# Performance work log

Measured on AMD Instinct MI355X. Metric: run time of the kernel, lower is better.

## Reference

```python
import jax, jax.numpy as jnp
import numpy as np

P = 7            # pooling_size
SCALE = 1.0 / 16  # spatial_scale


def _roi_align(feat, tf):
    # feat: [B,C,T,H,W] (L2-normalized), tf: [N,7] = [b, x1, y1, t1, x2, y2, t2]
    # RoIAlignAvg with temporal pooled size == T (identity in time): bilinear
    # sample at each spatial bin center for every frame.
    H, W = feat.shape[-2], feat.shape[-1]
    b = tf[:, 0].astype(jnp.int32)
    x1, y1 = tf[:, 1] * SCALE, tf[:, 2] * SCALE
    x2, y2 = tf[:, 4] * SCALE, tf[:, 5] * SCALE
    bw = jnp.maximum(x2 - x1 + SCALE, 1e-3) / P
    bh = jnp.maximum(y2 - y1 + SCALE, 1e-3) / P
    ctr = jnp.arange(P, dtype=feat.dtype) + 0.5
    xs = jnp.clip(x1[:, None] + ctr * bw[:, None], 0.0, W - 1)  # [N,P]
    ys = jnp.clip(y1[:, None] + ctr * bh[:, None], 0.0, H - 1)  # [N,P]
    x0 = jnp.floor(xs); y0 = jnp.floor(ys)
    fx = xs - x0; fy = ys - y0
    x0i = x0.astype(jnp.int32); x1i = jnp.minimum(x0i + 1, W - 1)
    y0i = y0.astype(jnp.int32); y1i = jnp.minimum(y0i + 1, H - 1)

    def g(yi, xi):
        # advanced indices broadcast to [N,P,P]; result [N,P,P,C,T]
        return feat[b[:, None, None], :, :, yi[:, :, None], xi[:, None, :]]

    wy0 = (1 - fy)[:, :, None, None, None]; wy1 = fy[:, :, None, None, None]
    wx0 = (1 - fx)[:, None, :, None, None]; wx1 = fx[:, None, :, None, None]
    out = (wy0 * wx0 * g(y0i, x0i) + wy0 * wx1 * g(y0i, x1i)
           + wy1 * wx0 * g(y1i, x0i) + wy1 * wx1 * g(y1i, x1i))
    return jnp.transpose(out, (0, 3, 4, 1, 2))  # [N,C,T,P,P]


def _forward(base_feat, tubes, gt_rois, gt_tubes, conv_w, conv_b, w1, b1, w2, b2, wp, bp):
    B, C, T = base_feat.shape[:3]
    R = tubes.shape[1]
    # F.normalize(base_feat, p=2, dim=1)
    feat = base_feat / jnp.maximum(
        jnp.linalg.norm(base_feat, axis=1, keepdims=True), 1e-12)

    # --- ragged scatter: rois[b,i,t1:t2+1,1:] = tubes[b,i,[1,2,4,5]] ---
    f = jnp.arange(T)
    f_off = (f[None, :] + jnp.arange(B)[:, None] * T).astype(tubes.dtype)  # [B,T]
    t1 = tubes[..., 3].astype(jnp.int32)[..., None]
    t2 = tubes[..., 6].astype(jnp.int32)[..., None]
    mask = (f[None, None, :] >= t1) & (f[None, None, :] <= t2)  # [B,R,T]
    box = tubes[..., jnp.array([1, 2, 4, 5])]                   # [B,R,4]
    rois_box = jnp.where(mask[..., None], box[:, :, None, :],
                         jnp.zeros((), tubes.dtype))
    rois = jnp.concatenate(
        [jnp.broadcast_to(f_off[:, None, :, None], (B, R, T, 1)), rois_box], -1)

    # --- RoIAlign + AvgPool3d over T + head (eval mode: dropout = identity) ---
    pooled = _roi_align(feat, tubes.reshape(-1, 7))  # [N,C,T,P,P]
    pooled = pooled.mean(axis=2)                     # [N,C,P,P]
    x = jnp.einsum('nchw,oc->nohw', pooled, conv_w) + conv_b[None, :, None, None]
    x = x.reshape(x.shape[0], -1)                    # [N, C*P*P]
    x = jax.nn.relu(x @ w1 + b1)
    x = jax.nn.relu(x @ w2 + b2)
    bbox_pred = x @ wp + bp                          # [N, 4*T]
    return bbox_pred, pooled, rois


def setup_inputs() -> dict:
    B, R, T, C, HF, IMG = 4, 64, 16, 256, 14, 224
    ks = jax.random.split(jax.random.key(0), 16)
    base_feat = jax.random.normal(ks[0], (B, C, T, HF, HF), jnp.float32)
    x1 = jax.random.uniform(ks[1], (B, R), minval=0.0, maxval=IMG / 2)
    y1 = jax.random.uniform(ks[2], (B, R), minval=0.0, maxval=IMG / 2)
    x2 = jnp.minimum(x1 + jax.random.uniform(ks[3], (B, R), minval=16.0, maxval=IMG / 2), IMG - 1.0)
    y2 = jnp.minimum(y1 + jax.random.uniform(ks[4], (B, R), minval=16.0, maxval=IMG / 2), IMG - 1.0)
    tt = jax.random.randint(ks[5], (B, R, 2), 0, T)
    t1 = jnp.min(tt, -1).astype(jnp.float32)
    t2 = jnp.max(tt, -1).astype(jnp.float32)
    bidx = jnp.broadcast_to(jnp.arange(B)[:, None], (B, R)).astype(jnp.float32)
    tubes = jnp.stack([bidx, x1, y1, t1, x2, y2, t2], -1)
    s = 0.02
    return {
        'base_feat': base_feat,
        'tubes': tubes,
        'gt_rois': jax.random.normal(ks[6], (B, 10, T, 5), jnp.float32),
        'gt_tubes': jax.random.normal(ks[7], (B, 10, 7), jnp.float32),
        'conv_w': jax.random.normal(ks[8], (C, C), jnp.float32) * s,
        'conv_b': jnp.zeros((C,), jnp.float32),
        'w1': jax.random.normal(ks[9], (C * P * P, 2048), jnp.float32) * s,
        'b1': jnp.zeros((2048,), jnp.float32),
        'w2': jax.random.normal(ks[10], (2048, 512), jnp.float32) * s,
        'b2': jnp.zeros((512,), jnp.float32),
        'wp': jax.random.normal(ks[11], (512, 4 * T), jnp.float32) * s,
        'bp': jnp.zeros((4 * T,), jnp.float32),
    }


def reference(base_feat, tubes, gt_rois, gt_tubes, conv_w, conv_b, w1, b1, w2, b2, wp, bp):
    return _forward(base_feat, tubes, gt_rois, gt_tubes, conv_w, conv_b, w1, b1, w2, b2, wp, bp)
```

## Files before the change

kernel.cpp:

```cpp
#include <hip/hip_runtime.h>

#define HH 14
#define WW 14
#define HWSZ 196
#define TT 16
#define CC 256
#define BB 4
#define RR 64
#define NROI 256
#define PP 7
#define PP2 49

typedef short s4v __attribute__((ext_vector_type(4)));
typedef short s8v __attribute__((ext_vector_type(8)));
typedef float f4v __attribute__((ext_vector_type(4)));

__device__ inline ushort f2bf(float f) {
    union { float f; unsigned u; } v; v.f = f;
    unsigned r = v.u + 0x7fffu + ((v.u >> 16) & 1u);
    return (ushort)(r >> 16);
}

__global__ void k_sumsq(const float* __restrict__ base, float* __restrict__ partial) {
    int blk = blockIdx.x;
    int bt = blk >> 3, cg = blk & 7;
    int hw = threadIdx.x;
    if (hw >= HWSZ) return;
    int b = bt >> 4, t = bt & 15;
    const float* p = base + ((size_t)(b * CC + cg * 32) * TT + t) * HWSZ + hw;
    float s = 0.f;
    #pragma unroll 8
    for (int c = 0; c < 32; ++c) {
        float v = p[(size_t)c * TT * HWSZ];
        s += v * v;
    }
    partial[cg * 12544 + bt * HWSZ + hw] = s;
}

__global__ void k_finish_inv(const float* __restrict__ partial, float* __restrict__ inv) {
    int j = blockIdx.x * 256 + threadIdx.x;
    if (j >= 12544) return;
    float s = 0.f;
    #pragma unroll
    for (int cg = 0; cg < 8; ++cg) s += partial[cg * 12544 + j];
    inv[j] = 1.0f / fmaxf(sqrtf(s), 1e-12f);
}

__global__ void k_tsum(const float* __restrict__ base, const float* __restrict__ inv,
                       float* __restrict__ tsum) {
    int bc = blockIdx.x;
    int hw = threadIdx.x;
    if (hw >= HWSZ) return;
    int b = bc >> 8;
    const float* p = base + (size_t)bc * TT * HWSZ + hw;
    const float* iv = inv + b * TT * HWSZ + hw;
    float s = 0.f;
    #pragma unroll
    for (int t = 0; t < TT; ++t) s += p[t * HWSZ] * iv[t * HWSZ];
    tsum[(size_t)bc * HWSZ + hw] = s;
}

__global__ void k_rois(const float* __restrict__ tubes, float* __restrict__ rois) {
    int idx = blockIdx.x * 256 + threadIdx.x;
    if (idx >= BB * RR * TT) return;
    int t = idx & 15;
    int br = idx >> 4;
    int b = br >> 6;
    const float* tb = tubes + br * 7;
    int t1 = (int)tb[3], t2 = (int)tb[6];
    bool m = (t >= t1) && (t <= t2);
    float* o = rois + (size_t)idx * 5;
    o[0] = (float)(b * TT + t);
    o[1] = m ? tb[1] : 0.f;
    o[2] = m ? tb[2] : 0.f;
    o[3] = m ? tb[4] : 0.f;
    o[4] = m ? tb[5] : 0.f;
}

__global__ void k_roialign(const float* __restrict__ tubes, const float* __restrict__ tsum,
                           float* __restrict__ pooled, float* __restrict__ pooledT) {
    __shared__ int sx0[PP], sx1[PP], sy0[PP], sy1[PP];
    __shared__ float sfx[PP], sfy[PP];
    __shared__ int sb;
    int n = blockIdx.x;
    int tid = threadIdx.x;
    if (tid < PP) {
        const float* tb = tubes + n * 7;
        float x1 = tb[1] * 0.0625f, y1 = tb[2] * 0.0625f;
        float x2 = tb[4] * 0.0625f, y2 = tb[5] * 0.0625f;
        float bw = fmaxf(x2 - x1 + 0.0625f, 0.001f) * (1.0f / PP);
        float bh = fmaxf(y2 - y1 + 0.0625f, 0.001f) * (1.0f / PP);
        float ctr = tid + 0.5f;
        float xs = fminf(fmaxf(x1 + ctr * bw, 0.f), (float)(WW - 1));
        float ys = fminf(fmaxf(y1 + ctr * bh, 0.f), (float)(HH - 1));
        float x0f = floorf(xs), y0f = floorf(ys);
        int x0 = (int)x0f, y0 = (int)y0f;
        sx0[tid] = x0; sx1[tid] = min(x0 + 1, WW - 1);
        sy0[tid] = y0; sy1[tid] = min(y0 + 1, HH - 1);
        sfx[tid] = xs - x0f; sfy[tid] = ys - y0f;
        if (tid == 0) sb = (int)tb[0];
    }
    __syncthreads();
    const float* tbase = tsum + (size_t)sb * CC * HWSZ;
    for (int idx = tid; idx < CC * PP2; idx += 256) {
        int c = idx / PP2, bin = idx % PP2;
        int py = bin / PP, px = bin % PP;
        const float* tp = tbase + (size_t)c * HWSZ;
        float fx = sfx[px], fy = sfy[py];
        int y0 = sy0[py] * WW, y1 = sy1[py] * WW;
        float v00 = tp[y0 + sx0[px]];
        float v01 = tp[y0 + sx1[px]];
        float v10 = tp[y1 + sx0[px]];
        float v11 = tp[y1 + sx1[px]];
        float v = (1.f - fy) * ((1.f - fx) * v00 + fx * v01)
                + fy        * ((1.f - fx) * v10 + fx * v11);
        v *= (1.0f / TT);
        pooled[(size_t)n * CC * PP2 + idx] = v;
        pooledT[((size_t)n * PP2 + bin) * CC + c] = v;
    }
}

__global__ __launch_bounds__(256) void gemm64(const float* __restrict__ A,
                                              const float* __restrict__ B_,
                                              float* __restrict__ Cp,
                                              int M, int N, int K,
                                              int lda, int ldb, int kChunk) {
    __shared__ float As[16][64];
    __shared__ float Bs[16][68];
    int m0 = blockIdx.x * 64, n0 = blockIdx.y * 64;
    int s = blockIdx.z;
    int k0 = s * kChunk, kend = k0 + kChunk;
    int tid = threadIdx.x;
    int am = tid >> 2, ak = (tid & 3) << 2;
    int bk = tid >> 4, bn = (tid & 15) << 2;
    int tm = tid >> 4, tn = tid & 15;
    float acc[4][4] = {};
    const float* Aptr = A + (size_t)(m0 + am) * lda + ak;
    const float* Bptr = B_ + (size_t)bk * ldb + n0 + bn;

    for (int kk = k0; kk < kend; kk += 16) {
        float4 av = *(const float4*)(Aptr + kk);
        float4 bv = *(const float4*)(Bptr + (size_t)kk * ldb);
        __syncthreads();
        As[ak + 0][am] = av.x;
        As[ak + 1][am] = av.y;
        As[ak + 2][am] = av.z;
        As[ak + 3][am] = av.w;
        *(float4*)&Bs[bk][bn] = bv;
        __syncthreads();
        #pragma unroll
        for (int k = 0; k < 16; ++k) {
            float4 a = *(const float4*)&As[k][tm << 2];
            float4 b = *(const float4*)&Bs[k][tn << 2];
            float a4[4] = {a.x, a.y, a.z, a.w};
            float b4[4] = {b.x, b.y, b.z, b.w};
            #pragma unroll
            for (int i = 0; i < 4; ++i)
                #pragma unroll
                for (int j = 0; j < 4; ++j)
                    acc[i][j] += a4[i] * b4[j];
        }
    }
    float* Cs = Cp + (size_t)s * M * N;
    #pragma unroll
    for (int i = 0; i < 4; ++i) {
        float4 v = make_float4(acc[i][0], acc[i][1], acc[i][2], acc[i][3]);
        *(float4*)&Cs[(size_t)(m0 + (tm << 2) + i) * N + n0 + (tn << 2)] = v;
    }
}

__global__ void k_reduce(const float* __restrict__ part, const float* __restrict__ bias,
                         float* __restrict__ out, int MN, int N, int S, int relu) {
    int idx = blockIdx.x * 256 + threadIdx.x;
    if (idx >= MN) return;
    float s = bias[idx % N];
    for (int i = 0; i < S; ++i) s += part[(size_t)i * MN + idx];
    if (relu) s = fmaxf(s, 0.f);
    out[idx] = s;
}

__global__ __launch_bounds__(512) void conv_mfma(const float* __restrict__ pooledT,
                                                 const float* __restrict__ conv_w,
                                                 const float* __restrict__ conv_b,
                                                 float* __restrict__ x) {
    __shared__ __align__(16) ushort Ab[2][8192];
    __shared__ __align__(16) ushort Bres[8192];
    const int m0 = blockIdx.x * 256, o0 = blockIdx.y * 64;
    const int tid = threadIdx.x;
    const int lane = tid & 63, w = tid >> 6;
    const int wm = w & 3, wn = w >> 2;
    const int fr = lane & 15, fg = lane >> 4;

    for (int ii = tid; ii < 2048; ii += 512) {
        int o_l = ii >> 5, cq = ii & 31;
        const float* s = conv_w + (size_t)(o0 + o_l) * 256 + cq * 8;
        float4 v0 = *(const float4*)s;
        float4 v1 = *(const float4*)(s + 4);
        float vv[8] = {v0.x, v0.y, v0.z, v0.w, v1.x, v1.y, v1.z, v1.w};
        int dbase = (cq >> 2) * 2048 + (o_l >> 4) * 512 + (cq & 3) * 128 + (o_l & 15);
        #pragma unroll
        for (int jc = 0; jc < 8; ++jc) Bres[dbase + jc * 16] = f2bf(vv[jc]);
    }

    int ii0 = tid, ii1 = 512 + tid, ii2 = 1024 + tid, ii3 = 1536 + tid;
    const float* pA0 = pooledT + (size_t)(m0 + (ii0 >> 3)) * 256 + (ii0 & 7) * 4;
    const float* pA1 = pooledT + (size_t)(m0 + (ii1 >> 3)) * 256 + (ii1 & 7) * 4;
    const float* pA2 = pooledT + (size_t)(m0 + (ii2 >> 3)) * 256 + (ii2 & 7) * 4;
    const float* pA3 = pooledT + (size_t)(m0 + (ii3 >> 3)) * 256 + (ii3 & 7) * 4;
#define CDOFF(ii) (((ii >> 3) >> 4) * 512 + ((ii & 7) >> 1) * 128 + ((ii >> 3) & 15) * 8 + (ii & 1) * 4)
    const int do0 = CDOFF(ii0), do1 = CDOFF(ii1), do2 = CDOFF(ii2), do3 = CDOFF(ii3);
#undef CDOFF
    float4 a0_, a1_, a2_, a3_;
#define CONV_LOAD(t) do { a0_ = *(const float4*)(pA0 + (t) * 32); \
                          a1_ = *(const float4*)(pA1 + (t) * 32); \
                          a2_ = *(const float4*)(pA2 + (t) * 32); \
                          a3_ = *(const float4*)(pA3 + (t) * 32); } while (0)
#define W4(dst, v) do { s4v _u; _u[0]=(short)f2bf((v).x); _u[1]=(short)f2bf((v).y); \
                        _u[2]=(short)f2bf((v).z); _u[3]=(short)f2bf((v).w); \
                        *(s4v*)(dst) = _u; } while (0)
#define CONV_WRITE(buf) do { W4(Ab[buf] + do0, a0_); W4(Ab[buf] + do1, a1_); \
                             W4(Ab[buf] + do2, a2_); W4(Ab[buf] + do3, a3_); } while (0)

    CONV_LOAD(0);
    CONV_WRITE(0);
    __syncthreads();

    const int aoff = wm * 2048 + fg * 128 + fr * 8;
    f4v acc[4][2];
    #pragma unroll
    for (int i = 0; i < 4; ++i)
        #pragma unroll
        for (int j = 0; j < 2; ++j) acc[i][j] = (f4v){0.f, 0.f, 0.f, 0.f};

    for (int t = 0; t < 8; ++t) {
        if (t < 7) CONV_LOAD(t + 1);
        const ushort* A = Ab[t & 1];
        s8v a0 = *(const s8v*)(A + aoff);
        s8v a1 = *(const s8v*)(A + aoff + 512);
        s8v a2 = *(const s8v*)(A + aoff + 1024);
        s8v a3 = *(const s8v*)(A + aoff + 1536);
        unsigned bbase = (unsigned)(size_t)(&Bres[0]) + t * 4096 + wn * 2048 + fg * 256 + fr * 2;
        s4v bl0, bh0, bl1, bh1;
        asm volatile("ds_read_b64_tr_b16 %0, %2\n\t"
                     "ds_read_b64_tr_b16 %1, %2 offset:128"
                     : "=v"(bl0), "=v"(bh0) : "v"(bbase));
        asm volatile("ds_read_b64_tr_b16 %0, %2 offset:1024\n\t"
                     "ds_read_b64_tr_b16 %1, %2 offset:1152"
                     : "=v"(bl1), "=v"(bh1) : "v"(bbase));
        asm volatile("s_waitcnt lgkmcnt(0)" ::: "memory");
        __builtin_amdgcn_sched_barrier(0);
        s8v b0, b1;
        b0[0] = bl0[0]; b0[1] = bl0[1]; b0[2] = bl0[2]; b0[3] = bl0[3];
        b0[4] = bh0[0]; b0[5] = bh0[1]; b0[6] = bh0[2]; b0[7] = bh0[3];
        b1[0] = bl1[0]; b1[1] = bl1[1]; b1[2] = bl1[2]; b1[3] = bl1[3];
        b1[4] = bh1[0]; b1[5] = bh1[1]; b1[6] = bh1[2]; b1[7] = bh1[3];
        acc[0][0] = __builtin_amdgcn_mfma_f32_16x16x32_bf16(a0, b0, acc[0][0], 0, 0, 0);
        acc[0][1] = __builtin_amdgcn_mfma_f32_16x16x32_bf16(a0, b1, acc[0][1], 0, 0, 0);
        acc[1][0] = __builtin_amdgcn_mfma_f32_16x16x32_bf16(a1, b0, acc[1][0], 0, 0, 0);
        acc[1][1] = __builtin_amdgcn_mfma_f32_16x16x32_bf16(a1, b1, acc[1][1], 0, 0, 0);
        acc[2][0] = __builtin_amdgcn_mfma_f32_16x16x32_bf16(a2, b0, acc[2][0], 0, 0, 0);
        acc[2][1] = __builtin_amdgcn_mfma_f32_16x16x32_bf16(a2, b1, acc[2][1], 0, 0, 0);
        acc[3][0] = __builtin_amdgcn_mfma_f32_16x16x32_bf16(a3, b0, acc[3][0], 0, 0, 0);
        acc[3][1] = __builtin_amdgcn_mfma_f32_16x16x32_bf16(a3, b1, acc[3][1], 0, 0, 0);
        if (t < 7) CONV_WRITE((t + 1) & 1);
        __syncthreads();
    }
#undef CONV_LOAD
#undef CONV_WRITE
#undef W4

    #pragma unroll
    for (int ni = 0; ni < 2; ++ni) {
        int o = o0 + wn * 32 + ni * 16 + fr;
        float cb = conv_b[o];
        #pragma unroll
        for (int mi = 0; mi < 4; ++mi)
            #pragma unroll
            for (int i = 0; i < 4; ++i) {
                int gm = m0 + wm * 64 + mi * 16 + fg * 4 + i;
                int n = gm / 49;
                int hw = gm - n * 49;
                x[(size_t)n * 12544 + o * 49 + hw] = acc[mi][ni][i] + cb;
            }
    }
}

__global__ void k_cvt_x(const float* __restrict__ x, ushort* __restrict__ xb) {
    int idx = blockIdx.x * 256 + threadIdx.x;
    if (idx >= 256 * 1568) return;
    int kg = idx >> 10;
    int r = idx & 1023;
    int rblk = r >> 6, q = (r >> 4) & 3, fr = r & 15;
    int m = rblk * 16 + fr;
    const float* src = x + (size_t)m * 12544 + kg * 32 + q * 8;
    float4 v0 = *(const float4*)src;
    float4 v1 = *(const float4*)(src + 4);
    ushort o[8] = {f2bf(v0.x), f2bf(v0.y), f2bf(v0.z), f2bf(v0.w),
                   f2bf(v1.x), f2bf(v1.y), f2bf(v1.z), f2bf(v1.w)};
    *(s8v*)(xb + (size_t)idx * 8) = *(s8v*)o;
}

__global__ __launch_bounds__(512) void fc1_mfma(const ushort* __restrict__ xb,
                                                const float* __restrict__ w1,
                                                float* __restrict__ part) {
    __shared__ __align__(16) ushort Ab[4][8192];
    __shared__ __align__(16) ushort Bbf[2][2048];
    const int nblk = blockIdx.x, s = blockIdx.y;
    const int n0 = nblk * 64;
    const int k0 = s * 1568;
    const int tid = threadIdx.x;
    const int lane = tid & 63, w = tid >> 6;
    const int wm = w & 3, wn = w >> 2;
    const int fr = lane & 15, fg = lane >> 4;

    const ushort* gA = xb + (size_t)s * 49 * 8192;
    const int slot0 = tid, slot1 = 512 + tid;

    const int kr = (w >> 2) * 16 + (lane >> 2);
    const int bnb = w & 3, bnq = lane & 3;
    const float* gB = w1 + (size_t)(k0 + kr) * 2048 + n0 + bnb * 16 + bnq * 4;
    const int bw_u = bnb * 512 + kr * 16 + bnq * 4;

    const int aoff = wm * 2048 + fg * 128 + fr * 8;
    f4v acc[4][2];
    #pragma unroll
    for (int i = 0; i < 4; ++i)
        #pragma unroll
        for (int j = 0; j < 2; ++j) acc[i][j] = (f4v){0.f, 0.f, 0.f, 0.f};

#define STAGE_A(buf, kg) do {                                                                   \
    ushort* _d = Ab[buf];                                                                       \
    __builtin_amdgcn_global_load_lds(                                                           \
        (const __attribute__((address_space(1))) void*)(gA + (size_t)(kg) * 8192 + slot0 * 8),  \
        (__attribute__((address_space(3))) void*)(_d + slot0 * 8), 16, 0, 0);                   \
    __builtin_amdgcn_global_load_lds(                                                           \
        (const __attribute__((address_space(1))) void*)(gA + (size_t)(kg) * 8192 + slot1 * 8),  \
        (__attribute__((address_space(3))) void*)(_d + slot1 * 8), 16, 0, 0);                   \
} while (0)
#define GBP(t) (*(const float4*)(gB + (size_t)(t) * 65536))
#define BWRITE(buf, rb) do {                                                                    \
    s4v _u; _u[0] = (short)f2bf((rb).x); _u[1] = (short)f2bf((rb).y);                           \
    _u[2] = (short)f2bf((rb).z); _u[3] = (short)f2bf((rb).w);                                   \
    *(s4v*)&Bbf[buf][bw_u] = _u;                                                                \
} while (0)

    float4 rb0, rb1, rb2, rb3;
    STAGE_A(0, 0);
    STAGE_A(1, 1);
    rb0 = GBP(0); rb1 = GBP(1); rb2 = GBP(2); rb3 = GBP(3);
    BWRITE(0, rb0);
    __builtin_amdgcn_sched_barrier(0);
    asm volatile("s_waitcnt vmcnt(3) lgkmcnt(0)" ::: "memory");
    __builtin_amdgcn_s_barrier();
    __builtin_amdgcn_sched_barrier(0);

#define FC1_BODY(t, rbL, rbU) do {                                                              \
    int kg2 = (t) + 2 > 48 ? 48 : (t) + 2;                                                      \
    int kg4 = (t) + 4 > 48 ? 48 : (t) + 4;                                                      \
    STAGE_A(((t) + 2) & 3, kg2);                                                                \
    __builtin_amdgcn_sched_barrier(0);                                                          \
    rbL = GBP(kg4);                                                                             \
    __builtin_amdgcn_sched_barrier(0);                                                          \
    const ushort* _A = Ab[(t) & 3];                                                             \
    s8v _a0 = *(const s8v*)(_A + aoff);                                                         \
    s8v _a1 = *(const s8v*)(_A + aoff + 512);                                                   \
    s8v _a2 = *(const s8v*)(_A + aoff + 1024);                                                  \
    s8v _a3 = *(const s8v*)(_A + aoff + 1536);                                                  \
    unsigned _bb = (unsigned)(size_t)(&Bbf[(t) & 1][0]) + wn * 2048 + fg * 256 + fr * 2;        \
    s4v _bl0, _bh0, _bl1, _bh1;                                                                 \
    asm volatile("ds_read_b64_tr_b16 %0, %2\n\t"                                                \
                 "ds_read_b64_tr_b16 %1, %2 offset:128"                                         \
                 : "=v"(_bl0), "=v"(_bh0) : "v"(_bb));                                          \
    asm volatile("ds_read_b64_tr_b16 %0, %2 offset:1024\n\t"                                    \
                 "ds_read_b64_tr_b16 %1, %2 offset:1152"                                        \
                 : "=v"(_bl1), "=v"(_bh1) : "v"(_bb));                                          \
    asm volatile("s_waitcnt lgkmcnt(0)" ::: "memory");                                          \
    __builtin_amdgcn_sched_barrier(0);                                                          \
    s8v _b0, _b1;                                                                               \
    _b0[0]=_bl0[0]; _b0[1]=_bl0[1]; _b0[2]=_bl0[2]; _b0[3]=_bl0[3];                             \
    _b0[4]=_bh0[0]; _b0[5]=_bh0[1]; _b0[6]=_bh0[2]; _b0[7]=_bh0[3];                             \
    _b1[0]=_bl1[0]; _b1[1]=_bl1[1]; _b1[2]=_bl1[2]; _b1[3]=_bl1[3];                             \
    _b1[4]=_bh1[0]; _b1[5]=_bh1[1]; _b1[6]=_bh1[2]; _b1[7]=_bh1[3];                             \
    acc[0][0] = __builtin_amdgcn_mfma_f32_16x16x32_bf16(_a0, _b0, acc[0][0], 0, 0, 0);          \
    acc[0][1] = __builtin_amdgcn_mfma_f32_16x16x32_bf16(_a0, _b1, acc[0][1], 0, 0, 0);          \
    acc[1][0] = __builtin_amdgcn_mfma_f32_16x16x32_bf16(_a1, _b0, acc[1][0], 0, 0, 0);          \
    acc[1][1] = __builtin_amdgcn_mfma_f32_16x16x32_bf16(_a1, _b1, acc[1][1], 0, 0, 0);          \
    acc[2][0] = __builtin_amdgcn_mfma_f32_16x16x32_bf16(_a2, _b0, acc[2][0], 0, 0, 0);          \
    acc[2][1] = __builtin_amdgcn_mfma_f32_16x16x32_bf16(_a2, _b1, acc[2][1], 0, 0, 0);          \
    acc[3][0] = __builtin_amdgcn_mfma_f32_16x16x32_bf16(_a3, _b0, acc[3][0], 0, 0, 0);          \
    acc[3][1] = __builtin_amdgcn_mfma_f32_16x16x32_bf16(_a3, _b1, acc[3][1], 0, 0, 0);          \
    BWRITE(((t) + 1) & 1, rbU);                                                                 \
    __builtin_amdgcn_sched_barrier(0);                                                          \
    asm volatile("s_waitcnt vmcnt(4) lgkmcnt(0)" ::: "memory");                                 \
    __builtin_amdgcn_s_barrier();                                                               \
    __builtin_amdgcn_sched_barrier(0);                                                          \
} while (0)

    for (int tb = 0; tb < 44; tb += 4) {
        FC1_BODY(tb + 0, rb0, rb1);
        FC1_BODY(tb + 1, rb1, rb2);
        FC1_BODY(tb + 2, rb2, rb3);
        FC1_BODY(tb + 3, rb3, rb0);
    }
    FC1_BODY(44, rb0, rb1);
    FC1_BODY(45, rb1, rb2);
    FC1_BODY(46, rb2, rb3);
    FC1_BODY(47, rb3, rb0);

    {
        const ushort* _A = Ab[0];
        s8v _a0 = *(const s8v*)(_A + aoff);
        s8v _a1 = *(const s8v*)(_A + aoff + 512);
        s8v _a2 = *(const s8v*)(_A + aoff + 1024);
        s8v _a3 = *(const s8v*)(_A + aoff + 1536);
        unsigned _bb = (unsigned)(size_t)(&Bbf[0][0]) + wn * 2048 + fg * 256 + fr * 2;
        s4v _bl0, _bh0, _bl1, _bh1;
        asm volatile("ds_read_b64_tr_b16 %0, %2\n\t"
                     "ds_read_b64_tr_b16 %1, %2 offset:128"
                     : "=v"(_bl0), "=v"(_bh0) : "v"(_bb));
        asm volatile("ds_read_b64_tr_b16 %0, %2 offset:1024\n\t"
                     "ds_read_b64_tr_b16 %1, %2 offset:1152"
                     : "=v"(_bl1), "=v"(_bh1) : "v"(_bb));
        asm volatile("s_waitcnt lgkmcnt(0)" ::: "memory");
        __builtin_amdgcn_sched_barrier(0);
        s8v _b0, _b1;
        _b0[0]=_bl0[0]; _b0[1]=_bl0[1]; _b0[2]=_bl0[2]; _b0[3]=_bl0[3];
        _b0[4]=_bh0[0]; _b0[5]=_bh0[1]; _b0[6]=_bh0[2]; _b0[7]=_bh0[3];
        _b1[0]=_bl1[0]; _b1[1]=_bl1[1]; _b1[2]=_bl1[2]; _b1[3]=_bl1[3];
        _b1[4]=_bh1[0]; _b1[5]=_bh1[1]; _b1[6]=_bh1[2]; _b1[7]=_bh1[3];
        acc[0][0] = __builtin_amdgcn_mfma_f32_16x16x32_bf16(_a0, _b0, acc[0][0], 0, 0, 0);
        acc[0][1] = __builtin_amdgcn_mfma_f32_16x16x32_bf16(_a0, _b1, acc[0][1], 0, 0, 0);
        acc[1][0] = __builtin_amdgcn_mfma_f32_16x16x32_bf16(_a1, _b0, acc[1][0], 0, 0, 0);
        acc[1][1] = __builtin_amdgcn_mfma_f32_16x16x32_bf16(_a1, _b1, acc[1][1], 0, 0, 0);
        acc[2][0] = __builtin_amdgcn_mfma_f32_16x16x32_bf16(_a2, _b0, acc[2][0], 0, 0, 0);
        acc[2][1] = __builtin_amdgcn_mfma_f32_16x16x32_bf16(_a2, _b1, acc[2][1], 0, 0, 0);
        acc[3][0] = __builtin_amdgcn_mfma_f32_16x16x32_bf16(_a3, _b0, acc[3][0], 0, 0, 0);
        acc[3][1] = __builtin_amdgcn_mfma_f32_16x16x32_bf16(_a3, _b1, acc[3][1], 0, 0, 0);
    }
#undef FC1_BODY
#undef STAGE_A
#undef GBP
#undef BWRITE

    float* dst = part + (size_t)s * 256 * 2048 + n0 + wn * 32 + fr;
    #pragma unroll
    for (int mi = 0; mi < 4; ++mi)
        #pragma unroll
        for (int ni = 0; ni < 2; ++ni)
            #pragma unroll
            for (int i = 0; i < 4; ++i) {
                int row = wm * 64 + mi * 16 + fg * 4 + i;
                dst[(size_t)row * 2048 + ni * 16] = acc[mi][ni][i];
            }
}

extern "C" void kernel_launch(void* const* d_in, const int* in_sizes, int n_in,
                              void* d_out, int out_size, void* d_ws, size_t ws_size,
                              hipStream_t stream) {
    const float* base   = (const float*)d_in[0];
    const float* tubes  = (const float*)d_in[1];
    const float* conv_w = (const float*)d_in[4];
    const float* conv_b = (const float*)d_in[5];
    const float* w1     = (const float*)d_in[6];
    const float* b1     = (const float*)d_in[7];
    const float* w2     = (const float*)d_in[8];
    const float* b2     = (const float*)d_in[9];
    const float* wp     = (const float*)d_in[10];
    const float* bp     = (const float*)d_in[11];

    float* out    = (float*)d_out;
    float* bbox   = out;
    float* pooled = out + 16384;
    float* rois   = out + 16384 + 3211264;

    float* ws      = (float*)d_ws;
    float* inv     = ws;
    float* partial = ws + 12544;
    float* tsum    = ws + 112896;
    float* pooledT = ws + 313600;
    float* x       = ws + 3524864;
    float* h1      = ws + 6736128;
    float* h2      = ws + 7260416;
    float* part    = ws + 7391488;
    ushort* xb     = (ushort*)pooledT;

    k_sumsq<<<BB * TT * 8, 256, 0, stream>>>(base, partial);
    k_finish_inv<<<49, 256, 0, stream>>>(partial, inv);
    k_tsum<<<BB * CC, 256, 0, stream>>>(base, inv, tsum);
    k_rois<<<(BB * RR * TT + 255) / 256, 256, 0, stream>>>(tubes, rois);
    k_roialign<<<NROI, 256, 0, stream>>>(tubes, tsum, pooled, pooledT);

    conv_mfma<<<dim3(49, 4), 512, 0, stream>>>(pooledT, conv_w, conv_b, x);

    k_cvt_x<<<1568, 256, 0, stream>>>(x, xb);

    fc1_mfma<<<dim3(32, 8), 512, 0, stream>>>(xb, w1, part);
    k_reduce<<<(256 * 2048 + 255) / 256, 256, 0, stream>>>(part, b1, h1, 256 * 2048, 2048, 8, 1);

    gemm64<<<dim3(4, 8, 8), 256, 0, stream>>>(h1, w2, part,
                                              256, 512, 2048, 2048, 512, 256);
    k_reduce<<<(256 * 512 + 255) / 256, 256, 0, stream>>>(part, b2, h2, 256 * 512, 512, 8, 1);

    gemm64<<<dim3(4, 1, 8), 256, 0, stream>>>(h2, wp, part,
                                              256, 64, 512, 512, 64, 64);
    k_reduce<<<(256 * 64 + 255) / 256, 256, 0, stream>>>(part, bp, bbox, 256 * 64, 64, 8, 0);
}
```

Before: 133.3 us.

## Fuse rois into roialign, write bf16 fc1 operand from conv, drop k_cvt_x

The rois scatter moves into the RoIAlign kernel, and RoIAlign splits its work into two loops so that both the pooled and pooledT stores are coalesced. The conv epilogue writes bf16 directly in the fc1 operand layout, ordered hw-major. fc1 then gathers w1 rows with a matching permuted k index, which removes the separate conversion kernel and its fp32 intermediate round trip. fc1 grid axes are also swapped. The cost is a second bilinear pass in RoIAlign, scattered 2-byte stores in the conv epilogue, and noncontiguous w1 row reads in fc1.

```diff
diff --git a/kernel.cpp b/kernel.cpp
--- a/kernel.cpp
+++ b/kernel.cpp
@@ -60,25 +60,9 @@
     tsum[(size_t)bc * HWSZ + hw] = s;
 }
 
-__global__ void k_rois(const float* __restrict__ tubes, float* __restrict__ rois) {
-    int idx = blockIdx.x * 256 + threadIdx.x;
-    if (idx >= BB * RR * TT) return;
-    int t = idx & 15;
-    int br = idx >> 4;
-    int b = br >> 6;
-    const float* tb = tubes + br * 7;
-    int t1 = (int)tb[3], t2 = (int)tb[6];
-    bool m = (t >= t1) && (t <= t2);
-    float* o = rois + (size_t)idx * 5;
-    o[0] = (float)(b * TT + t);
-    o[1] = m ? tb[1] : 0.f;
-    o[2] = m ? tb[2] : 0.f;
-    o[3] = m ? tb[4] : 0.f;
-    o[4] = m ? tb[5] : 0.f;
-}
-
 __global__ void k_roialign(const float* __restrict__ tubes, const float* __restrict__ tsum,
-                           float* __restrict__ pooled, float* __restrict__ pooledT) {
+                           float* __restrict__ pooled, float* __restrict__ pooledT,
+                           float* __restrict__ rois) {
     __shared__ int sx0[PP], sx1[PP], sy0[PP], sy1[PP];
     __shared__ float sfx[PP], sfy[PP];
     __shared__ int sb;
@@ -100,11 +84,24 @@
         sfx[tid] = xs - x0f; sfy[tid] = ys - y0f;
         if (tid == 0) sb = (int)tb[0];
     }
+    if (tid < TT) {
+        const float* tb = tubes + n * 7;
+        int t1 = (int)tb[3], t2 = (int)tb[6];
+        bool m = (tid >= t1) && (tid <= t2);
+        int b = n >> 6;
+        float* o = rois + ((size_t)n * TT + tid) * 5;
+        o[0] = (float)(b * TT + tid);
+        o[1] = m ? tb[1] : 0.f;
+        o[2] = m ? tb[2] : 0.f;
+        o[3] = m ? tb[4] : 0.f;
+        o[4] = m ? tb[5] : 0.f;
+    }
     __syncthreads();
     const float* tbase = tsum + (size_t)sb * CC * HWSZ;
+
     for (int idx = tid; idx < CC * PP2; idx += 256) {
-        int c = idx / PP2, bin = idx % PP2;
-        int py = bin / PP, px = bin % PP;
+        int c = idx / PP2, bin = idx - (idx / PP2) * PP2;
+        int py = bin / PP, px = bin - (bin / PP) * PP;
         const float* tp = tbase + (size_t)c * HWSZ;
         float fx = sfx[px], fy = sfy[py];
         int y0 = sy0[py] * WW, y1 = sy1[py] * WW;
@@ -114,9 +111,21 @@
         float v11 = tp[y1 + sx1[px]];
         float v = (1.f - fy) * ((1.f - fx) * v00 + fx * v01)
                 + fy        * ((1.f - fx) * v10 + fx * v11);
-        v *= (1.0f / TT);
-        pooled[(size_t)n * CC * PP2 + idx] = v;
-        pooledT[((size_t)n * PP2 + bin) * CC + c] = v;
+        pooled[(size_t)n * CC * PP2 + idx] = v * (1.0f / TT);
+    }
+    for (int idx = tid; idx < PP2 * CC; idx += 256) {
+        int bin = idx >> 8, c = idx & 255;
+        int py = bin / PP, px = bin - (bin / PP) * PP;
+        const float* tp = tbase + (size_t)c * HWSZ;
+        float fx = sfx[px], fy = sfy[py];
+        int y0 = sy0[py] * WW, y1 = sy1[py] * WW;
+        float v00 = tp[y0 + sx0[px]];
+        float v01 = tp[y0 + sx1[px]];
+        float v10 = tp[y1 + sx0[px]];
+        float v11 = tp[y1 + sx1[px]];
+        float v = (1.f - fy) * ((1.f - fx) * v00 + fx * v01)
+                + fy        * ((1.f - fx) * v10 + fx * v11);
+        pooledT[((size_t)n * PP2 + bin) * CC + c] = v * (1.0f / TT);
     }
 }
 
@@ -182,7 +191,7 @@
 __global__ __launch_bounds__(512) void conv_mfma(const float* __restrict__ pooledT,
                                                  const float* __restrict__ conv_w,
                                                  const float* __restrict__ conv_b,
-                                                 float* __restrict__ x) {
+                                                 ushort* __restrict__ xb) {
     __shared__ __align__(16) ushort Ab[2][8192];
     __shared__ __align__(16) ushort Bres[8192];
     const int m0 = blockIdx.x * 256, o0 = blockIdx.y * 64;
@@ -273,31 +282,17 @@
     for (int ni = 0; ni < 2; ++ni) {
         int o = o0 + wn * 32 + ni * 16 + fr;
         float cb = conv_b[o];
+        int obase = (o >> 5) * 8192 + (((o >> 3) & 3)) * 128 + (o & 7);
         #pragma unroll
         for (int mi = 0; mi < 4; ++mi)
             #pragma unroll
             for (int i = 0; i < 4; ++i) {
                 int gm = m0 + wm * 64 + mi * 16 + fg * 4 + i;
-                int n = gm / 49;
-                int hw = gm - n * 49;
-                x[(size_t)n * 12544 + o * 49 + hw] = acc[mi][ni][i] + cb;
+                int n = gm / 49, hw = gm - n * 49;
+                xb[(size_t)hw * 65536 + obase + (n >> 4) * 512 + (n & 15) * 8]
+                    = f2bf(acc[mi][ni][i] + cb);
             }
     }
-}
-
-__global__ void k_cvt_x(const float* __restrict__ x, ushort* __restrict__ xb) {
-    int idx = blockIdx.x * 256 + threadIdx.x;
-    if (idx >= 256 * 1568) return;
-    int kg = idx >> 10;
-    int r = idx & 1023;
-    int rblk = r >> 6, q = (r >> 4) & 3, fr = r & 15;
-    int m = rblk * 16 + fr;
-    const float* src = x + (size_t)m * 12544 + kg * 32 + q * 8;
-    float4 v0 = *(const float4*)src;
-    float4 v1 = *(const float4*)(src + 4);
-    ushort o[8] = {f2bf(v0.x), f2bf(v0.y), f2bf(v0.z), f2bf(v0.w),
-                   f2bf(v1.x), f2bf(v1.y), f2bf(v1.z), f2bf(v1.w)};
-    *(s8v*)(xb + (size_t)idx * 8) = *(s8v*)o;
 }
 
 __global__ __launch_bounds__(512) void fc1_mfma(const ushort* __restrict__ xb,
@@ -305,7 +300,7 @@
                                                 float* __restrict__ part) {
     __shared__ __align__(16) ushort Ab[4][8192];
     __shared__ __align__(16) ushort Bbf[2][2048];
-    const int nblk = blockIdx.x, s = blockIdx.y;
+    const int s = blockIdx.x, nblk = blockIdx.y;
     const int n0 = nblk * 64;
     const int k0 = s * 1568;
     const int tid = threadIdx.x;
@@ -318,7 +313,7 @@
 
     const int kr = (w >> 2) * 16 + (lane >> 2);
     const int bnb = w & 3, bnq = lane & 3;
-    const float* gB = w1 + (size_t)(k0 + kr) * 2048 + n0 + bnb * 16 + bnq * 4;
+    const int ncol = n0 + bnb * 16 + bnq * 4;
     const int bw_u = bnb * 512 + kr * 16 + bnq * 4;
 
     const int aoff = wm * 2048 + fg * 128 + fr * 8;
@@ -337,7 +332,9 @@
         (const __attribute__((address_space(1))) void*)(gA + (size_t)(kg) * 8192 + slot1 * 8),  \
         (__attribute__((address_space(3))) void*)(_d + slot1 * 8), 16, 0, 0);                   \
 } while (0)
-#define GBP(t) (*(const float4*)(gB + (size_t)(t) * 65536))
+#define GBP(t) (*(const float4*)(w1 +                                                           \
+    (size_t)(((unsigned)(k0 + (t) * 32 + kr) & 255u) * 49 +                                     \
+             ((unsigned)(k0 + (t) * 32 + kr) >> 8)) * 2048 + ncol))
 #define BWRITE(buf, rb) do {                                                                    \
     s4v _u; _u[0] = (short)f2bf((rb).x); _u[1] = (short)f2bf((rb).y);                           \
     _u[2] = (short)f2bf((rb).z); _u[3] = (short)f2bf((rb).w);                                   \
@@ -478,23 +475,19 @@
     float* partial = ws + 12544;
     float* tsum    = ws + 112896;
     float* pooledT = ws + 313600;
-    float* x       = ws + 3524864;
+    ushort* xb     = (ushort*)(ws + 3524864);
     float* h1      = ws + 6736128;
     float* h2      = ws + 7260416;
     float* part    = ws + 7391488;
-    ushort* xb     = (ushort*)pooledT;
 
     k_sumsq<<<BB * TT * 8, 256, 0, stream>>>(base, partial);
     k_finish_inv<<<49, 256, 0, stream>>>(partial, inv);
     k_tsum<<<BB * CC, 256, 0, stream>>>(base, inv, tsum);
-    k_rois<<<(BB * RR * TT + 255) / 256, 256, 0, stream>>>(tubes, rois);
-    k_roialign<<<NROI, 256, 0, stream>>>(tubes, tsum, pooled, pooledT);
-
-    conv_mfma<<<dim3(49, 4), 512, 0, stream>>>(pooledT, conv_w, conv_b, x);
-
-    k_cvt_x<<<1568, 256, 0, stream>>>(x, xb);
-
-    fc1_mfma<<<dim3(32, 8), 512, 0, stream>>>(xb, w1, part);
+    k_roialign<<<NROI, 256, 0, stream>>>(tubes, tsum, pooled, pooledT, rois);
+
+    conv_mfma<<<dim3(49, 4), 512, 0, stream>>>(pooledT, conv_w, conv_b, xb);
+
+    fc1_mfma<<<dim3(8, 32), 512, 0, stream>>>(xb, w1, part);
     k_reduce<<<(256 * 2048 + 255) / 256, 256, 0, stream>>>(part, b1, h1, 256 * 2048, 2048, 8, 1);
 
     gemm64<<<dim3(4, 8, 8), 256, 0, stream>>>(h1, w2, part,
```

New measurement: 125.9 us. -5.6%, faster.
